# Optimization experiments

Hardware: AMD Instinct MI355X
Metric: run time of the kernel (lower is better)

The kernel has to match this reference:

```python
import jax, jax.numpy as jnp
import numpy as np

N_NODES = 25000
N_EDGES = 400000
D_FEAT = 128
HIDDEN = 64
HEADS = 4


def _segment_softmax(logits, segment_ids, num_segments):
    # numerically stable softmax over variable-size neighborhoods
    seg_max = jax.ops.segment_max(logits, segment_ids, num_segments=num_segments)
    ex = jnp.exp(logits - seg_max[segment_ids])
    seg_sum = jax.ops.segment_sum(ex, segment_ids, num_segments=num_segments)
    return ex / seg_sum[segment_ids]


def _gat_layer(nodes, senders, receivers, Wq, bq, Wl, bl, last):
    n = nodes.shape[0]
    h = (nodes @ Wq + bq)[:, :, None]            # [N, hidden, 1] (query fn + expand_dims)
    sent = h[senders]                            # [E, hidden, 1]
    recv = h[receivers]                          # [E, hidden, 1]
    cat = jnp.concatenate([sent, recv], axis=-1) # [E, hidden, 2]
    logits = jax.nn.leaky_relu(cat @ Wl + bl, negative_slope=0.2)  # [E, hidden, heads]
    w = _segment_softmax(logits, receivers, n)   # [E, hidden, heads]
    msgs = sent * w                              # broadcast over heads
    agg = jax.ops.segment_sum(msgs, receivers, num_segments=n)     # [N, hidden, heads]
    if last:
        return jax.nn.elu(agg.mean(axis=-1))     # [N, hidden]
    return jax.nn.elu(agg.reshape(n, -1))        # [N, hidden*heads]


def setup_inputs() -> dict:
    key = jax.random.key(0)
    ks = jax.random.split(key, 16)
    d1 = HIDDEN * HEADS
    inp = {
        "nodes": jax.random.normal(ks[0], (N_NODES, D_FEAT), dtype=jnp.float32),
        "senders": jax.random.randint(ks[1], (N_EDGES,), 0, N_NODES, dtype=jnp.int64)
        if jax.config.jax_enable_x64 else jax.random.randint(ks[1], (N_EDGES,), 0, N_NODES).astype(jnp.int32),
        "receivers": jax.random.randint(ks[2], (N_EDGES,), 0, N_NODES).astype(jnp.int32),
        "Wq0": jax.random.normal(ks[3], (D_FEAT, HIDDEN), dtype=jnp.float32) / np.sqrt(D_FEAT),
        "bq0": jnp.zeros((HIDDEN,), jnp.float32),
        "Wl0": jax.random.normal(ks[4], (2, HEADS), dtype=jnp.float32) / np.sqrt(2.0),
        "bl0": jnp.zeros((HEADS,), jnp.float32),
        "Wq1": jax.random.normal(ks[5], (d1, HIDDEN), dtype=jnp.float32) / np.sqrt(d1),
        "bq1": jnp.zeros((HIDDEN,), jnp.float32),
        "Wl1": jax.random.normal(ks[6], (2, HEADS), dtype=jnp.float32) / np.sqrt(2.0),
        "bl1": jnp.zeros((HEADS,), jnp.float32),
        "Wq2": jax.random.normal(ks[7], (d1, HIDDEN), dtype=jnp.float32) / np.sqrt(d1),
        "bq2": jnp.zeros((HIDDEN,), jnp.float32),
        "Wl2": jax.random.normal(ks[8], (2, HEADS), dtype=jnp.float32) / np.sqrt(2.0),
        "bl2": jnp.zeros((HEADS,), jnp.float32),
    }
    inp["senders"] = inp["senders"].astype(jnp.int32)
    return inp


def reference(nodes, senders, receivers, Wq0, bq0, Wl0, bl0, Wq1, bq1, Wl1, bl1, Wq2, bq2, Wl2, bl2):
    x = _gat_layer(nodes, senders, receivers, Wq0, bq0, Wl0, bl0, last=False)
    x = _gat_layer(x, senders, receivers, Wq1, bq1, Wl1, bl1, last=False)
    x = _gat_layer(x, senders, receivers, Wq2, bq2, Wl2, bl2, last=True)
    return x
```

## Files before the change

kernel.cpp:

```cpp
#include <hip/hip_runtime.h>
#include <hip/hip_bf16.h>

#define HID 64
#define HEADS 4

typedef short s16x8 __attribute__((ext_vector_type(8)));
typedef short s16x4 __attribute__((ext_vector_type(4)));
typedef float f32x4 __attribute__((ext_vector_type(4)));
typedef float f32x2 __attribute__((ext_vector_type(2)));

__device__ __forceinline__ float ldw(const void* p, long i, bool f32) {
    return f32 ? ((const float*)p)[i] : (float)((const __hip_bfloat16*)p)[i];
}

__device__ __forceinline__ unsigned short f2b(float f) {
    unsigned int u = __builtin_bit_cast(unsigned int, f);
    u += 0x7FFF + ((u >> 16) & 1);
    return (unsigned short)(u >> 16);
}
__device__ __forceinline__ float b2f(unsigned short s) {
    unsigned int u = ((unsigned int)s) << 16;
    return __builtin_bit_cast(float, u);
}
__device__ __forceinline__ short f2h(float f) {
    return __builtin_bit_cast(short, (_Float16)f);
}

#if __has_builtin(__builtin_amdgcn_exp2f)
#define EXP2(x) __builtin_amdgcn_exp2f(x)
#else
#define EXP2(x) exp2f(x)
#endif
#if __has_builtin(__builtin_amdgcn_rcpf)
#define RCP(x) __builtin_amdgcn_rcpf(x)
#else
#define RCP(x) (1.0f / (x))
#endif

__device__ __forceinline__ void edge_softmax(
    const _Float16* __restrict__ hbp, int sv, int cR,
    const f32x2 (&w0p)[2], const f32x2 (&cp)[2],
    f32x2 (&lp)[2], f32x2 (&ap)[2]) {
    #define LD(j) hbp[(long)(__builtin_amdgcn_readlane(sv, (j)) * HID)]
    #define STEP(hc) {                                                     \
        float _h = (float)(hc);                       \
        _Pragma("unroll")                                                  \
        for (int q = 0; q < 2; q++) {                                      \
            f32x2 t = w0p[q] * _h + cp[q];                                 \
            f32x2 u = t * 0.2f;                                            \
            t.x = fmaxf(t.x, u.x); t.y = fmaxf(t.y, u.y);                  \
            f32x2 pe; pe.x = EXP2(t.x); pe.y = EXP2(t.y);                  \
            lp[q] += pe;                                                   \
            ap[q] += pe * _h;                                              \
        } }

    _Float16 q0 = LD(0), q1 = LD(1), q2 = LD(2), q3 = LD(3);
    _Float16 q4 = LD(4), q5 = LD(5), q6 = LD(6), q7 = LD(7);
    int j = 0;
    for (; j + 8 <= cR; j += 8) {
        _Float16 a0 = q0, a1 = q1, a2 = q2, a3 = q3;
        _Float16 a4 = q4, a5 = q5, a6 = q6, a7 = q7;
        if (j + 8 < 64) {
            q0 = LD(j +  8); q1 = LD(j +  9); q2 = LD(j + 10); q3 = LD(j + 11);
            q4 = LD(j + 12); q5 = LD(j + 13); q6 = LD(j + 14); q7 = LD(j + 15);
        }
        STEP(a0); STEP(a1); STEP(a2); STEP(a3);
        STEP(a4); STEP(a5); STEP(a6); STEP(a7);
    }
    int remn = cR - j;
    if (remn > 0) STEP(q0);
    if (remn > 1) STEP(q1);
    if (remn > 2) STEP(q2);
    if (remn > 3) STEP(q3);
    if (remn > 4) STEP(q4);
    if (remn > 5) STEP(q5);
    if (remn > 6) STEP(q6);
    #undef LD
    #undef STEP
}

__global__ __launch_bounds__(256) void prep_kernel(
    const void* __restrict__ nodes,
    const void* __restrict__ W0, const void* __restrict__ W1, const void* __restrict__ W2,
    const void* __restrict__ Wl0, const void* __restrict__ bl0,
    const void* __restrict__ Wl1, const void* __restrict__ bl1,
    const void* __restrict__ Wl2, const void* __restrict__ bl2,
    int* __restrict__ flag_out,
    unsigned short* __restrict__ T0, unsigned short* __restrict__ T1,
    unsigned short* __restrict__ T2, float* __restrict__ Wlp,
    int* __restrict__ cnt, int N64) {
    __shared__ int sflag;
    if (threadIdx.x == 0) sflag = 0;
    __syncthreads();
    {
        const uint4* pw = (const uint4*)nodes;
        int hits = 0;
        for (int i = threadIdx.x; i < 2048; i += 256) {
            uint4 u = pw[i];
            unsigned int w[4] = {u.x, u.y, u.z, u.w};
            #pragma unroll
            for (int j = 0; j < 4; j++) {
                if ((w[j] & 0x7F80u) == 0x7F80u) hits++;
                if (((w[j] >> 16) & 0x7F80u) == 0x7F80u) hits++;
            }
        }
        if (__ballot(hits != 0)) { if ((threadIdx.x & 63) == 0) sflag = 1; }
    }
    __syncthreads();
    const bool f32 = (sflag != 0);
    if (blockIdx.x == 0 && threadIdx.x == 0) *flag_out = f32 ? 100 : 0;

    int g = blockIdx.x * 256 + threadIdx.x;
    int stride = gridDim.x * 256;

    for (int i = g; i < N64; i += stride) cnt[i] = 0;

    for (int i = g; i < 40960; i += stride) {
        int k, n;
        if (i < 8192) {
            k = i >> 6; n = i & 63;
            T0[n * 128 + k] = f32 ? f2b(((const float*)W0)[i])
                                  : ((const unsigned short*)W0)[i];
        } else {
            const void* W; unsigned short* T; int o;
            if (i < 24576) { W = W1; T = T1; o = i - 8192; }
            else           { W = W2; T = T2; o = i - 24576; }
            k = o >> 6; n = o & 63;
            float w = ldw(W, o, f32);
            T[n * 256 + k] = f32 ? f2b(w) : (unsigned short)f2h(w);
        }
    }
    if (blockIdx.x == 0 && threadIdx.x < 48) {
        int L = threadIdx.x >> 4, s = threadIdx.x & 15;
        const void* W = (L == 0) ? Wl0 : ((L == 1) ? Wl1 : Wl2);
        const void* B = (L == 0) ? bl0 : ((L == 1) ? bl1 : bl2);
        float v = 0.f;
        if (s < 8)       v = ldw(W, s, f32);
        else if (s < 12) v = ldw(B, s - 8, f32);
        Wlp[L * 16 + s] = v * 1.44269504f;
    }
}

template <int K, int AMODE>
__device__ __forceinline__ void gemm_body(const unsigned short* __restrict__ Ah,
                                          const unsigned short* __restrict__ Al,
                                          const unsigned short* __restrict__ Wt,
                                          const void* __restrict__ bq,
                                          bool f32,
                                          _Float16* __restrict__ h, int M, int blockId) {
    constexpr int KP = K + 8;
    __shared__ __align__(16) unsigned short Ws[64 * KP];
    int tid = threadIdx.x;
    #pragma unroll
    for (int it = 0; it < (64 * K) / 2048; it++) {
        int i = it * 2048 + tid * 8;
        int row = i / K, col = i % K;
        *(s16x8*)&Ws[row * KP + col] = *(const s16x8*)(Wt + i);
    }
    __syncthreads();

    int lane = tid & 63, wv = tid >> 6;
    int m16 = lane & 15, quad = lane >> 4;

    int tiles = (M + 15) >> 4;
    int tile = blockId * 4 + wv;
    if (tile >= tiles) return;

    float bias[4];
    #pragma unroll
    for (int t = 0; t < 4; t++) bias[t] = ldw(bq, 16 * t + m16, f32);

    int m0 = tile << 4;
    int row = m0 + m16;
    bool rv = row < M;
    long abase = (long)row * K;
    f32x4 acc[4] = {{0.f,0.f,0.f,0.f},{0.f,0.f,0.f,0.f},{0.f,0.f,0.f,0.f},{0.f,0.f,0.f,0.f}};

    #pragma unroll
    for (int ks = 0; ks < K / 32; ks++) {
        int kb = ks * 32 + quad * 8;
        s16x8 b[4];
        #pragma unroll
        for (int t = 0; t < 4; t++)
            b[t] = *(const s16x8*)&Ws[(16 * t + m16) * KP + kb];
        if (AMODE == 3) {
            const float* Af = (const float*)Ah;
            f32x4 v0 = {0.f,0.f,0.f,0.f}, v1 = {0.f,0.f,0.f,0.f};
            if (rv) {
                v0 = *(const f32x4*)(Af + abase + kb);
                v1 = *(const f32x4*)(Af + abase + kb + 4);
            }
            s16x8 ah, al;
            #pragma unroll
            for (int jj = 0; jj < 8; jj++) {
                float f = (jj < 4) ? v0[jj] : v1[jj - 4];
                unsigned short hb = f2b(f);
                ah[jj] = (short)hb;
                al[jj] = (short)f2b(f - b2f(hb));
            }
            #pragma unroll
            for (int t = 0; t < 4; t++)
                acc[t] = __builtin_amdgcn_mfma_f32_16x16x32_bf16(ah, b[t], acc[t], 0, 0, 0);
            #pragma unroll
            for (int t = 0; t < 4; t++)
                acc[t] = __builtin_amdgcn_mfma_f32_16x16x32_bf16(al, b[t], acc[t], 0, 0, 0);
        } else {
            s16x8 ah = rv ? *(const s16x8*)(Ah + abase + kb) : (s16x8){0,0,0,0,0,0,0,0};
            if (AMODE == 0) {
                #pragma unroll
                for (int t = 0; t < 4; t++)
                    acc[t] = __builtin_amdgcn_mfma_f32_16x16x32_bf16(ah, b[t], acc[t], 0, 0, 0);
            } else if (AMODE == 1) {
                #pragma unroll
                for (int t = 0; t < 4; t++)
                    acc[t] = __builtin_amdgcn_mfma_f32_16x16x32_f16(ah, b[t], acc[t], 0, 0, 0);
            } else {
                #pragma unroll
                for (int t = 0; t < 4; t++)
                    acc[t] = __builtin_amdgcn_mfma_f32_16x16x32_bf16(ah, b[t], acc[t], 0, 0, 0);
                s16x8 al = rv ? *(const s16x8*)(Al + abase + kb) : (s16x8){0,0,0,0,0,0,0,0};
                #pragma unroll
                for (int t = 0; t < 4; t++)
                    acc[t] = __builtin_amdgcn_mfma_f32_16x16x32_bf16(al, b[t], acc[t], 0, 0, 0);
            }
        }
    }

    #pragma unroll
    for (int t = 0; t < 4; t++) {
        #pragma unroll
        for (int r = 0; r < 4; r++) {
            int orow = m0 + quad * 4 + r;
            if (orow < M) h[(long)orow * 64 + 16 * t + m16] = (_Float16)(acc[t][r] + bias[t]);
        }
    }
}

template <int K>
__global__ __launch_bounds__(256) void gemm_mfma(const unsigned short* __restrict__ Ah,
                                                 const unsigned short* __restrict__ Al,
                                                 const unsigned short* __restrict__ Wt,
                                                 const void* __restrict__ bq,
                                                 const int* __restrict__ flag,
                                                 _Float16* __restrict__ h, int M) {
    const bool f32 = (*flag >= 8);
    if (f32) gemm_body<K, 2>(Ah, Al, Wt, bq, true, h, M, blockIdx.x);
    else     gemm_body<K, 1>(Ah, nullptr, Wt, bq, false, h, M, blockIdx.x);
}

__global__ __launch_bounds__(256) void gemm0_scatter(
    const void* __restrict__ nodes,
    const unsigned short* __restrict__ Wt, const void* __restrict__ bq,
    const int* __restrict__ flag, _Float16* __restrict__ h, int M,
    const int* __restrict__ recv, const int* __restrict__ send,
    int* __restrict__ cnt, unsigned short* __restrict__ slots, int E, int gemmBlocks) {
    if ((int)blockIdx.x < gemmBlocks) {
        const bool f32 = (*flag >= 8);
        if (f32) gemm_body<128, 3>((const unsigned short*)nodes, nullptr, Wt, bq,
                                   true, h, M, blockIdx.x);
        else     gemm_body<128, 0>((const unsigned short*)nodes, nullptr, Wt, bq,
                                   false, h, M, blockIdx.x);
    } else {
        int g = (blockIdx.x - gemmBlocks) * 256 + threadIdx.x;
        int stride = (gridDim.x - gemmBlocks) * 256;
        for (int i = g; i < E; i += stride) {
            int r = recv[i];
            int pos = atomicAdd(&cnt[r], 1);
            if (pos < 64) slots[r * 64 + pos] = (unsigned short)send[i];
        }
    }
}

__global__ __launch_bounds__(256) void attn_kernel(
    const _Float16* __restrict__ h, const int* __restrict__ cnt,
    const unsigned short* __restrict__ slots,
    const float* __restrict__ wlp,
    const int* __restrict__ flag,
    unsigned short* __restrict__ xh, unsigned short* __restrict__ xl,
    void* __restrict__ out, int n, int last) {
    const bool f32 = (*flag >= 8);
    int lane = threadIdx.x & 63;
    int r = __builtin_amdgcn_readfirstlane(blockIdx.x * 4 + (threadIdx.x >> 6));
    if (r >= n) return;

    int cR = cnt[r];
    cR = min(cR, 64);
    int sv = slots[r * 64 + lane];
    if (lane >= cR) sv = 0;

    float hr = (float)h[(long)r * HID + lane];
    f32x4 w0v = *(const f32x4*)(wlp);
    f32x4 w1v = *(const f32x4*)(wlp + 4);
    f32x4 bv  = *(const f32x4*)(wlp + 8);
    f32x2 w0p[2], cp[2];
    #pragma unroll
    for (int q = 0; q < 2; q++) {
        #pragma unroll
        for (int c = 0; c < 2; c++) {
            int k = 2 * q + c;
            w0p[q][c] = w0v[k];
            cp[q][c] = fmaf(hr, w1v[k], bv[k]);
        }
    }
    f32x2 lp[2] = {{0.f, 0.f}, {0.f, 0.f}};
    f32x2 ap[2] = {{0.f, 0.f}, {0.f, 0.f}};
    edge_softmax(h + lane, sv, cR, w0p, cp, lp, ap);

    bool has = (cR > 0);
    if (!last) {
        float v[4];
        #pragma unroll
        for (int k = 0; k < HEADS; k++) {
            float a = has ? ap[k >> 1][k & 1] * RCP(lp[k >> 1][k & 1]) : 0.f;
            v[k] = (a > 0.f) ? a : (__expf(a) - 1.f);
        }
        long o = (long)r * (HID * HEADS) + lane * HEADS;
        if (!f32) {
            s16x4 vf;
            #pragma unroll
            for (int k = 0; k < HEADS; k++) vf[k] = f2h(v[k]);
            *(s16x4*)(xh + o) = vf;
        } else {
            s16x4 vh, vlo;
            #pragma unroll
            for (int k = 0; k < HEADS; k++) {
                unsigned short hbk = f2b(v[k]);
                vh[k] = (short)hbk;
                vlo[k] = (short)f2b(v[k] - b2f(hbk));
            }
            *(s16x4*)(xh + o) = vh;
            *(s16x4*)(xl + o) = vlo;
        }
    } else {
        float s = 0.f;
        #pragma unroll
        for (int k = 0; k < HEADS; k++)
            s += has ? ap[k >> 1][k & 1] * RCP(lp[k >> 1][k & 1]) : 0.f;
        float a = s * 0.25f;
        a = (a > 0.f) ? a : (__expf(a) - 1.f);
        if (f32) ((float*)out)[(long)r * HID + lane] = a;
        else     ((__hip_bfloat16*)out)[(long)r * HID + lane] = (__hip_bfloat16)a;
    }
}


extern "C" void kernel_launch(void* const* d_in, const int* in_sizes, int n_in,
                              void* d_out, int out_size, void* d_ws, size_t ws_size,
                              hipStream_t stream) {
    const void* nodes    = d_in[0];
    const int* senders   = (const int*)d_in[1];
    const int* receivers = (const int*)d_in[2];
    const void* Wq0 = d_in[3];  const void* bq0 = d_in[4];
    const void* Wl0 = d_in[5];  const void* bl0 = d_in[6];
    const void* Wq1 = d_in[7];  const void* bq1 = d_in[8];
    const void* Wl1 = d_in[9];  const void* bl1 = d_in[10];
    const void* Wq2 = d_in[11]; const void* bq2 = d_in[12];
    const void* Wl2 = d_in[13]; const void* bl2 = d_in[14];

    int N = in_sizes[0] / 128;
    int E = in_sizes[1];
    int N64 = ((N + 63) / 64) * 64;

    char* p = (char*)d_ws;
    int* flag = (int*)p;            p += 64;
    _Float16* h = (_Float16*)p;     p += (size_t)N64 * 64 * 2;
    unsigned short* xh = (unsigned short*)p;  p += (size_t)N64 * 256 * 2;
    unsigned short* xl = (unsigned short*)p;  p += (size_t)N64 * 256 * 2;
    unsigned short* Wt0 = (unsigned short*)p; p += 128 * 64 * 2;
    unsigned short* Wt1 = (unsigned short*)p; p += 256 * 64 * 2;
    unsigned short* Wt2 = (unsigned short*)p; p += 256 * 64 * 2;
    float* Wlp = (float*)p;         p += 64 * 4;
    int* cnt = (int*)p;             p += (size_t)N64 * 4;
    unsigned short* slots = (unsigned short*)p; p += (size_t)N64 * 64 * 2;

    prep_kernel<<<64, 256, 0, stream>>>(nodes, Wq0, Wq1, Wq2,
                                        Wl0, bl0, Wl1, bl1, Wl2, bl2,
                                        flag, Wt0, Wt1, Wt2, Wlp, cnt, N64);

    int attnGrid = (N + 3) / 4;
    int tiles = (N + 15) / 16;
    int gemmGrid = (tiles + 3) / 4;

    gemm0_scatter<<<gemmGrid * 2, 256, 0, stream>>>(nodes, Wt0, bq0, flag, h, N,
                                                    receivers, senders, cnt, slots,
                                                    E, gemmGrid);
    attn_kernel<<<attnGrid, 256, 0, stream>>>(h, cnt, slots, Wlp + 0, flag,
                                              xh, xl, nullptr, N, 0);
    gemm_mfma<256><<<gemmGrid, 256, 0, stream>>>(xh, xl, Wt1, bq1, flag, h, N);
    attn_kernel<<<attnGrid, 256, 0, stream>>>(h, cnt, slots, Wlp + 16, flag,
                                              xh, xl, nullptr, N, 0);
    gemm_mfma<256><<<gemmGrid, 256, 0, stream>>>(xh, xl, Wt2, bq2, flag, h, N);
    attn_kernel<<<attnGrid, 256, 0, stream>>>(h, cnt, slots, Wlp + 32, flag,
                                              nullptr, nullptr, d_out, N, 1);
}
```

Before: 216.8 us.

## Split GEMM output columns across waves and drop shared-memory weight staging

Each wave now computes a 16x16 output slice (one of four column groups) instead of a full 16x64 tile, and B fragments are read straight from global/L2 rather than staged in LDS. The grid grows fourfold, which raises parallelism for the small node-feature GEMMs and removes the LDS fill and barrier. The scatter part gets a fixed block count, and the attention prefetch bound now uses the neighbour count, avoiding loads past the valid range. In exchange, A rows are reloaded by four waves and weights are fetched from cache without LDS reuse.

```diff
diff --git a/kernel.cpp b/kernel.cpp
--- a/kernel.cpp
+++ b/kernel.cpp
@@ -60,7 +60,7 @@
     for (; j + 8 <= cR; j += 8) {
         _Float16 a0 = q0, a1 = q1, a2 = q2, a3 = q3;
         _Float16 a4 = q4, a5 = q5, a6 = q6, a7 = q7;
-        if (j + 8 < 64) {
+        if (j + 8 < cR) {
             q0 = LD(j +  8); q1 = LD(j +  9); q2 = LD(j + 10); q3 = LD(j + 11);
             q4 = LD(j + 12); q5 = LD(j + 13); q6 = LD(j + 14); q7 = LD(j + 15);
         }
@@ -142,51 +142,34 @@
 }
 
 template <int K, int AMODE>
-__device__ __forceinline__ void gemm_body(const unsigned short* __restrict__ Ah,
+__device__ __forceinline__ void gemm_tile(const unsigned short* __restrict__ Ah,
                                           const unsigned short* __restrict__ Al,
                                           const unsigned short* __restrict__ Wt,
                                           const void* __restrict__ bq,
                                           bool f32,
-                                          _Float16* __restrict__ h, int M, int blockId) {
-    constexpr int KP = K + 8;
-    __shared__ __align__(16) unsigned short Ws[64 * KP];
-    int tid = threadIdx.x;
-    #pragma unroll
-    for (int it = 0; it < (64 * K) / 2048; it++) {
-        int i = it * 2048 + tid * 8;
-        int row = i / K, col = i % K;
-        *(s16x8*)&Ws[row * KP + col] = *(const s16x8*)(Wt + i);
-    }
-    __syncthreads();
-
-    int lane = tid & 63, wv = tid >> 6;
+                                          _Float16* __restrict__ h, int M, int wid) {
+    int tiles = (M + 15) >> 4;
+    int tile = wid >> 2, g = wid & 3;
+    if (tile >= tiles) return;
+    int lane = threadIdx.x & 63;
     int m16 = lane & 15, quad = lane >> 4;
-
-    int tiles = (M + 15) >> 4;
-    int tile = blockId * 4 + wv;
-    if (tile >= tiles) return;
-
-    float bias[4];
-    #pragma unroll
-    for (int t = 0; t < 4; t++) bias[t] = ldw(bq, 16 * t + m16, f32);
 
     int m0 = tile << 4;
     int row = m0 + m16;
     bool rv = row < M;
     long abase = (long)row * K;
-    f32x4 acc[4] = {{0.f,0.f,0.f,0.f},{0.f,0.f,0.f,0.f},{0.f,0.f,0.f,0.f},{0.f,0.f,0.f,0.f}};
+    const unsigned short* wrow = Wt + (16 * g + m16) * K;
+    float bias = ldw(bq, 16 * g + m16, f32);
+    f32x4 acc = {0.f, 0.f, 0.f, 0.f};
 
     #pragma unroll
     for (int ks = 0; ks < K / 32; ks++) {
         int kb = ks * 32 + quad * 8;
-        s16x8 b[4];
-        #pragma unroll
-        for (int t = 0; t < 4; t++)
-            b[t] = *(const s16x8*)&Ws[(16 * t + m16) * KP + kb];
+        s16x8 b = *(const s16x8*)(wrow + kb);
         if (AMODE == 3) {
-            const float* Af = (const float*)Ah;
             f32x4 v0 = {0.f,0.f,0.f,0.f}, v1 = {0.f,0.f,0.f,0.f};
             if (rv) {
+                const float* Af = (const float*)Ah;
                 v0 = *(const f32x4*)(Af + abase + kb);
                 v1 = *(const f32x4*)(Af + abase + kb + 4);
             }
@@ -198,41 +181,26 @@
                 ah[jj] = (short)hb;
                 al[jj] = (short)f2b(f - b2f(hb));
             }
-            #pragma unroll
-            for (int t = 0; t < 4; t++)
-                acc[t] = __builtin_amdgcn_mfma_f32_16x16x32_bf16(ah, b[t], acc[t], 0, 0, 0);
-            #pragma unroll
-            for (int t = 0; t < 4; t++)
-                acc[t] = __builtin_amdgcn_mfma_f32_16x16x32_bf16(al, b[t], acc[t], 0, 0, 0);
+            acc = __builtin_amdgcn_mfma_f32_16x16x32_bf16(ah, b, acc, 0, 0, 0);
+            acc = __builtin_amdgcn_mfma_f32_16x16x32_bf16(al, b, acc, 0, 0, 0);
         } else {
             s16x8 ah = rv ? *(const s16x8*)(Ah + abase + kb) : (s16x8){0,0,0,0,0,0,0,0};
             if (AMODE == 0) {
-                #pragma unroll
-                for (int t = 0; t < 4; t++)
-                    acc[t] = __builtin_amdgcn_mfma_f32_16x16x32_bf16(ah, b[t], acc[t], 0, 0, 0);
+                acc = __builtin_amdgcn_mfma_f32_16x16x32_bf16(ah, b, acc, 0, 0, 0);
             } else if (AMODE == 1) {
-                #pragma unroll
-                for (int t = 0; t < 4; t++)
-                    acc[t] = __builtin_amdgcn_mfma_f32_16x16x32_f16(ah, b[t], acc[t], 0, 0, 0);
+                acc = __builtin_amdgcn_mfma_f32_16x16x32_f16(ah, b, acc, 0, 0, 0);
             } else {
-                #pragma unroll
-                for (int t = 0; t < 4; t++)
-                    acc[t] = __builtin_amdgcn_mfma_f32_16x16x32_bf16(ah, b[t], acc[t], 0, 0, 0);
+                acc = __builtin_amdgcn_mfma_f32_16x16x32_bf16(ah, b, acc, 0, 0, 0);
                 s16x8 al = rv ? *(const s16x8*)(Al + abase + kb) : (s16x8){0,0,0,0,0,0,0,0};
-                #pragma unroll
-                for (int t = 0; t < 4; t++)
-                    acc[t] = __builtin_amdgcn_mfma_f32_16x16x32_bf16(al, b[t], acc[t], 0, 0, 0);
+                acc = __builtin_amdgcn_mfma_f32_16x16x32_bf16(al, b, acc, 0, 0, 0);
             }
         }
     }
 
     #pragma unroll
-    for (int t = 0; t < 4; t++) {
-        #pragma unroll
-        for (int r = 0; r < 4; r++) {
-            int orow = m0 + quad * 4 + r;
-            if (orow < M) h[(long)orow * 64 + 16 * t + m16] = (_Float16)(acc[t][r] + bias[t]);
-        }
+    for (int r = 0; r < 4; r++) {
+        int orow = m0 + quad * 4 + r;
+        if (orow < M) h[(long)orow * 64 + 16 * g + m16] = (_Float16)(acc[r] + bias);
     }
 }
 
@@ -244,8 +212,9 @@
                                                  const int* __restrict__ flag,
                                                  _Float16* __restrict__ h, int M) {
     const bool f32 = (*flag >= 8);
-    if (f32) gemm_body<K, 2>(Ah, Al, Wt, bq, true, h, M, blockIdx.x);
-    else     gemm_body<K, 1>(Ah, nullptr, Wt, bq, false, h, M, blockIdx.x);
+    int wid = blockIdx.x * 4 + (threadIdx.x >> 6);
+    if (f32) gemm_tile<K, 2>(Ah, Al, Wt, bq, true, h, M, wid);
+    else     gemm_tile<K, 1>(Ah, nullptr, Wt, bq, false, h, M, wid);
 }
 
 __global__ __launch_bounds__(256) void gemm0_scatter(
@@ -256,10 +225,11 @@
     int* __restrict__ cnt, unsigned short* __restrict__ slots, int E, int gemmBlocks) {
     if ((int)blockIdx.x < gemmBlocks) {
         const bool f32 = (*flag >= 8);
-        if (f32) gemm_body<128, 3>((const unsigned short*)nodes, nullptr, Wt, bq,
-                                   true, h, M, blockIdx.x);
-        else     gemm_body<128, 0>((const unsigned short*)nodes, nullptr, Wt, bq,
-                                   false, h, M, blockIdx.x);
+        int wid = blockIdx.x * 4 + (threadIdx.x >> 6);
+        if (f32) gemm_tile<128, 3>((const unsigned short*)nodes, nullptr, Wt, bq,
+                                   true, h, M, wid);
+        else     gemm_tile<128, 0>((const unsigned short*)nodes, nullptr, Wt, bq,
+                                   false, h, M, wid);
     } else {
         int g = (blockIdx.x - gemmBlocks) * 256 + threadIdx.x;
         int stride = (gridDim.x - gemmBlocks) * 256;
@@ -379,17 +349,17 @@
 
     int attnGrid = (N + 3) / 4;
     int tiles = (N + 15) / 16;
-    int gemmGrid = (tiles + 3) / 4;
-
-    gemm0_scatter<<<gemmGrid * 2, 256, 0, stream>>>(nodes, Wt0, bq0, flag, h, N,
-                                                    receivers, senders, cnt, slots,
-                                                    E, gemmGrid);
+    int scatBlocks = 392;
+
+    gemm0_scatter<<<tiles + scatBlocks, 256, 0, stream>>>(nodes, Wt0, bq0, flag, h, N,
+                                                          receivers, senders, cnt, slots,
+                                                          E, tiles);
     attn_kernel<<<attnGrid, 256, 0, stream>>>(h, cnt, slots, Wlp + 0, flag,
                                               xh, xl, nullptr, N, 0);
-    gemm_mfma<256><<<gemmGrid, 256, 0, stream>>>(xh, xl, Wt1, bq1, flag, h, N);
+    gemm_mfma<256><<<tiles, 256, 0, stream>>>(xh, xl, Wt1, bq1, flag, h, N);
     attn_kernel<<<attnGrid, 256, 0, stream>>>(h, cnt, slots, Wlp + 16, flag,
                                               xh, xl, nullptr, N, 0);
-    gemm_mfma<256><<<gemmGrid, 256, 0, stream>>>(xh, xl, Wt2, bq2, flag, h, N);
+    gemm_mfma<256><<<tiles, 256, 0, stream>>>(xh, xl, Wt2, bq2, flag, h, N);
     attn_kernel<<<attnGrid, 256, 0, stream>>>(h, cnt, slots, Wlp + 32, flag,
                                               nullptr, nullptr, d_out, N, 1);
 }
```

Result: slower. 245.8 us (+13.4%).
